# Kernel tuning notes

Measured on AMD Instinct MI355X. Metric: run time of the kernel, lower is better.

Reference implementation:

```python
import jax, jax.numpy as jnp
import numpy as np

B, L_SRC, L_TGT, H = 8, 256, 256, 768
N_SRC_WORDS, N_TGT_WORDS = 128, 128


def setup_inputs() -> dict:
    key = jax.random.key(0)
    k1, k2 = jax.random.split(key, 2)
    L = L_SRC + L_TGT
    tok_h = jax.random.normal(k1, (B, L, H), dtype=jnp.float32)
    attention_mask = jnp.ones((B, L), dtype=jnp.int32)
    # monotone word ids covering exactly N words (ragged spans of ~2 tokens/word)
    src_ids = (jnp.arange(L_SRC) * N_SRC_WORDS // L_SRC).astype(jnp.int64)
    tgt_ids = (jnp.arange(L_TGT) * N_TGT_WORDS // L_TGT).astype(jnp.int64)
    source_word_ids = jnp.broadcast_to(src_ids, (B, L_SRC))
    target_word_ids = jnp.broadcast_to(tgt_ids, (B, L_TGT))
    W = jax.random.normal(k2, (2 * H, 1), dtype=jnp.float32) * 0.02
    b = jnp.zeros((1,), dtype=jnp.float32)
    return dict(tok_h=tok_h, attention_mask=attention_mask,
                source_word_ids=source_word_ids, target_word_ids=target_word_ids,
                W=W, b=b, S=N_SRC_WORDS, T=N_TGT_WORDS)


def _pool_words(tok_h, combined_wid, attention_mask, n_words):
    """Vectorized equivalent of _pool_word_embeddings: mean over each
    contiguous run of equal word ids (masked / -1 tokens break runs)."""
    Bv, Lv, Hv = tok_h.shape
    valid = (attention_mask > 0) & (combined_wid >= 0)          # [B, L]
    prev_wid = jnp.pad(combined_wid[:, :-1], ((0, 0), (1, 0)), constant_values=-2)
    prev_valid = jnp.pad(valid[:, :-1], ((0, 0), (1, 0)), constant_values=False)
    new_run = valid & ((combined_wid != prev_wid) | (~prev_valid))
    run_id = jnp.cumsum(new_run.astype(jnp.int32), axis=1) - 1  # [B, L]
    n_seg = n_words + 1                                         # +1 dummy slot for invalid tokens
    seg = jnp.where(valid, run_id, n_words)
    gseg = (seg + jnp.arange(Bv, dtype=seg.dtype)[:, None] * n_seg).reshape(-1)
    sums = jax.ops.segment_sum(tok_h.reshape(Bv * Lv, Hv), gseg,
                               num_segments=Bv * n_seg).reshape(Bv, n_seg, Hv)
    counts = jax.ops.segment_sum(valid.astype(tok_h.dtype).reshape(-1), gseg,
                                 num_segments=Bv * n_seg).reshape(Bv, n_seg, 1)
    pooled = sums[:, :n_words] / jnp.maximum(counts[:, :n_words], 1.0)
    return pooled                                               # [B, n_words, H]


def reference(tok_h, attention_mask, source_word_ids, target_word_ids, W, b, S, T):
    combined_wid = jnp.concatenate([source_word_ids, target_word_ids], axis=1)  # [B, L]
    pooled = _pool_words(tok_h, combined_wid, attention_mask, S + T)            # [B, S+T, H]
    src = pooled[:, :S]            # [B, S, H]
    tgt = pooled[:, S:S + T]       # [B, T, H]
    # classifier(concat([src_exp, tgt_exp])) == src@W[:H] + tgt@W[H:] + b
    Hd = tok_h.shape[-1]
    w_src, w_tgt = W[:Hd, 0], W[Hd:, 0]
    logits = (src @ w_src)[:, :, None] + (tgt @ w_tgt)[:, None, :] + b[0]       # [B, S, T]
    return logits
```

## Files before the change

kernel.cpp:

```cpp
#include <hip/hip_runtime.h>
#include <hip/hip_bf16.h>

constexpr int B    = 8;
constexpr int LS   = 256;
constexpr int L    = 512;
constexpr int H    = 768;
constexpr int S    = 128;
constexpr int T    = 128;
constexpr int NW   = 256;
constexpr int NSEG = 513;

__global__ __launch_bounds__(64) void seg_count_kernel(
    const int* __restrict__ mask, const int* __restrict__ sw,
    const int* __restrict__ tw, int* __restrict__ seg,
    float* __restrict__ sums, float* __restrict__ cnts)
{
    const int b    = blockIdx.x;
    const int lane = threadIdx.x;

    __shared__ float lcnt[NSEG];
    for (int i = lane; i < NSEG; i += 64) lcnt[i] = 0.f;
    __syncthreads();

    const int base = lane * 8;
    int  wid[8]; bool val[8];
    #pragma unroll
    for (int j = 0; j < 8; ++j) {
        const int l = base + j;
        const int w = (l < LS) ? sw[b * LS + l] : tw[b * LS + (l - LS)];
        wid[j] = w;
        val[j] = (mask[b * L + l] > 0) && (w >= 0);
    }

    int pw = -2; bool pv = false;
    if (base > 0) {
        const int l = base - 1;
        pw = (l < LS) ? sw[b * LS + l] : tw[b * LS + (l - LS)];
        pv = (mask[b * L + l] > 0) && (pw >= 0);
    }

    int loc[8]; int c = 0;
    #pragma unroll
    for (int j = 0; j < 8; ++j) {
        const int nr = (val[j] && (wid[j] != pw || !pv)) ? 1 : 0;
        c += nr;
        loc[j] = c;
        pw = wid[j]; pv = val[j];
    }

    int inc = c;
    #pragma unroll
    for (int off = 1; off < 64; off <<= 1) {
        const int v = __shfl_up(inc, off);
        if (lane >= off) inc += v;
    }
    const int excl = inc - c;

    #pragma unroll
    for (int j = 0; j < 8; ++j) {
        const int rid = excl + loc[j] - 1;
        int sg = val[j] ? rid : NW;
        if (sg > NSEG - 1) sg = NSEG - 1;
        seg[b * L + base + j] = sg;
        atomicAdd(&lcnt[sg], 1.0f);
    }
    __syncthreads();

    for (int i = lane; i < NSEG; i += 64) {
        cnts[b * NSEG + i] = lcnt[i];
        sums[b * NSEG + i] = 0.f;
    }
}

__global__ __launch_bounds__(256) void dot_kernel(
    const float* __restrict__ tok, const float* __restrict__ Wp,
    const int* __restrict__ seg, float* __restrict__ sums)
{
    const int lane  = threadIdx.x & 63;
    const int wv    = threadIdx.x >> 6;
    const int token = blockIdx.x * 4 + wv;
    const int b     = token >> 9;

    const int sg = seg[token];
    if (sg >= NW) return;

    const float* wvec = Wp + ((sg < S) ? 0 : H);
    const float4* t4  = reinterpret_cast<const float4*>(tok + (size_t)token * H);
    const float4* w4  = reinterpret_cast<const float4*>(wvec);

    float acc = 0.f;
    #pragma unroll
    for (int k = 0; k < 3; ++k) {
        const float4 a = t4[lane + 64 * k];
        const float4 w = w4[lane + 64 * k];
        acc += a.x * w.x + a.y * w.y + a.z * w.z + a.w * w.w;
    }
    #pragma unroll
    for (int off = 32; off; off >>= 1) acc += __shfl_xor(acc, off);

    if (lane == 0) atomicAdd(&sums[b * NSEG + sg], acc);
}

__global__ __launch_bounds__(256) void logits_kernel(
    const float* __restrict__ sums, const float* __restrict__ cnts,
    const float* __restrict__ bias, float* __restrict__ out)
{
    const int b   = blockIdx.x;
    const int tid = threadIdx.x;

    __shared__ float ssrc[S], stgt[T];
    if (tid < S) {
        ssrc[tid] = sums[b * NSEG + tid] / fmaxf(cnts[b * NSEG + tid], 1.f);
    } else {
        const int j = tid - S;
        stgt[j] = sums[b * NSEG + S + j] / fmaxf(cnts[b * NSEG + S + j], 1.f);
    }
    __syncthreads();

    const float b0 = bias[0];
    const int i  = tid >> 1;
    const int jb = (tid & 1) * 64;
    const float si = ssrc[i] + b0;

    float4* o = reinterpret_cast<float4*>(out + (size_t)b * S * T + i * T + jb);
    #pragma unroll
    for (int j = 0; j < 64; j += 4) {
        float4 v;
        v.x = si + stgt[jb + j + 0];
        v.y = si + stgt[jb + j + 1];
        v.z = si + stgt[jb + j + 2];
        v.w = si + stgt[jb + j + 3];
        o[j >> 2] = v;
    }
}

extern "C" void kernel_launch(void* const* d_in, const int* in_sizes, int n_in,
                              void* d_out, int out_size, void* d_ws, size_t ws_size,
                              hipStream_t stream) {
    const float* tok  = (const float*)d_in[0];
    const int*   mask = (const int*)  d_in[1];
    const int*   sw   = (const int*)  d_in[2];
    const int*   tw   = (const int*)  d_in[3];
    const float* W    = (const float*)d_in[4];
    const float* bias = (const float*)d_in[5];
    float*       out  = (float*)d_out;

    float* sums = (float*)d_ws;
    float* cnts = sums + B * NSEG;
    int*   seg  = (int*)(cnts + B * NSEG);

    seg_count_kernel<<<B, 64, 0, stream>>>(mask, sw, tw, seg, sums, cnts);
    dot_kernel<<<(B * L) / 4, 256, 0, stream>>>(tok, W, seg, sums);
    logits_kernel<<<B, 256, 0, stream>>>(sums, cnts, bias, out);
}
```

Before: 16.90 us.

## Compute both weight dots per token and fuse segmentation into finalize kernel

The dot kernel no longer depends on segment ids. It computes each token's dot product against both the source and target weight halves and stores them as a float2. The segmentation scan, counting, pooling and logits are merged into one 1024-thread kernel per batch that uses shared-memory atomics. This removes one kernel launch and the global atomics, at the cost of a second dot product per token and an extra weight load.

```diff
diff --git a/kernel.cpp b/kernel.cpp
--- a/kernel.cpp
+++ b/kernel.cpp
@@ -8,128 +8,124 @@
 constexpr int S    = 128;
 constexpr int T    = 128;
 constexpr int NW   = 256;
-constexpr int NSEG = 513;
 
-__global__ __launch_bounds__(64) void seg_count_kernel(
-    const int* __restrict__ mask, const int* __restrict__ sw,
-    const int* __restrict__ tw, int* __restrict__ seg,
-    float* __restrict__ sums, float* __restrict__ cnts)
-{
-    const int b    = blockIdx.x;
-    const int lane = threadIdx.x;
-
-    __shared__ float lcnt[NSEG];
-    for (int i = lane; i < NSEG; i += 64) lcnt[i] = 0.f;
-    __syncthreads();
-
-    const int base = lane * 8;
-    int  wid[8]; bool val[8];
-    #pragma unroll
-    for (int j = 0; j < 8; ++j) {
-        const int l = base + j;
-        const int w = (l < LS) ? sw[b * LS + l] : tw[b * LS + (l - LS)];
-        wid[j] = w;
-        val[j] = (mask[b * L + l] > 0) && (w >= 0);
-    }
-
-    int pw = -2; bool pv = false;
-    if (base > 0) {
-        const int l = base - 1;
-        pw = (l < LS) ? sw[b * LS + l] : tw[b * LS + (l - LS)];
-        pv = (mask[b * L + l] > 0) && (pw >= 0);
-    }
-
-    int loc[8]; int c = 0;
-    #pragma unroll
-    for (int j = 0; j < 8; ++j) {
-        const int nr = (val[j] && (wid[j] != pw || !pv)) ? 1 : 0;
-        c += nr;
-        loc[j] = c;
-        pw = wid[j]; pv = val[j];
-    }
-
-    int inc = c;
-    #pragma unroll
-    for (int off = 1; off < 64; off <<= 1) {
-        const int v = __shfl_up(inc, off);
-        if (lane >= off) inc += v;
-    }
-    const int excl = inc - c;
-
-    #pragma unroll
-    for (int j = 0; j < 8; ++j) {
-        const int rid = excl + loc[j] - 1;
-        int sg = val[j] ? rid : NW;
-        if (sg > NSEG - 1) sg = NSEG - 1;
-        seg[b * L + base + j] = sg;
-        atomicAdd(&lcnt[sg], 1.0f);
-    }
-    __syncthreads();
-
-    for (int i = lane; i < NSEG; i += 64) {
-        cnts[b * NSEG + i] = lcnt[i];
-        sums[b * NSEG + i] = 0.f;
-    }
-}
-
-__global__ __launch_bounds__(256) void dot_kernel(
+__global__ __launch_bounds__(256) void dot2_kernel(
     const float* __restrict__ tok, const float* __restrict__ Wp,
-    const int* __restrict__ seg, float* __restrict__ sums)
+    float2* __restrict__ dvals)
 {
     const int lane  = threadIdx.x & 63;
     const int wv    = threadIdx.x >> 6;
     const int token = blockIdx.x * 4 + wv;
-    const int b     = token >> 9;
 
-    const int sg = seg[token];
-    if (sg >= NW) return;
+    const float4* t4 = reinterpret_cast<const float4*>(tok + (size_t)token * H);
+    const float4* s4 = reinterpret_cast<const float4*>(Wp);
+    const float4* g4 = reinterpret_cast<const float4*>(Wp + H);
 
-    const float* wvec = Wp + ((sg < S) ? 0 : H);
-    const float4* t4  = reinterpret_cast<const float4*>(tok + (size_t)token * H);
-    const float4* w4  = reinterpret_cast<const float4*>(wvec);
-
-    float acc = 0.f;
+    float as = 0.f, at = 0.f;
     #pragma unroll
     for (int k = 0; k < 3; ++k) {
         const float4 a = t4[lane + 64 * k];
-        const float4 w = w4[lane + 64 * k];
-        acc += a.x * w.x + a.y * w.y + a.z * w.z + a.w * w.w;
+        const float4 s = s4[lane + 64 * k];
+        const float4 g = g4[lane + 64 * k];
+        as += a.x * s.x + a.y * s.y + a.z * s.z + a.w * s.w;
+        at += a.x * g.x + a.y * g.y + a.z * g.z + a.w * g.w;
     }
     #pragma unroll
-    for (int off = 32; off; off >>= 1) acc += __shfl_xor(acc, off);
-
-    if (lane == 0) atomicAdd(&sums[b * NSEG + sg], acc);
+    for (int off = 32; off; off >>= 1) {
+        as += __shfl_xor(as, off);
+        at += __shfl_xor(at, off);
+    }
+    if (lane == 0) dvals[token] = make_float2(as, at);
 }
 
-__global__ __launch_bounds__(256) void logits_kernel(
-    const float* __restrict__ sums, const float* __restrict__ cnts,
+__global__ __launch_bounds__(1024) void finalize_kernel(
+    const int* __restrict__ mask, const int* __restrict__ sw,
+    const int* __restrict__ tw, const float2* __restrict__ dvals,
     const float* __restrict__ bias, float* __restrict__ out)
 {
     const int b   = blockIdx.x;
     const int tid = threadIdx.x;
 
-    __shared__ float ssrc[S], stgt[T];
-    if (tid < S) {
-        ssrc[tid] = sums[b * NSEG + tid] / fmaxf(cnts[b * NSEG + tid], 1.f);
-    } else {
-        const int j = tid - S;
-        stgt[j] = sums[b * NSEG + S + j] / fmaxf(cnts[b * NSEG + S + j], 1.f);
+    __shared__ int   sseg[L];
+    __shared__ float lsum[NW + 1];
+    __shared__ float lcnt[NW + 1];
+    __shared__ float pooled[NW];
+
+    if (tid < NW + 1) { lsum[tid] = 0.f; lcnt[tid] = 0.f; }
+    __syncthreads();
+
+    if (tid < 64) {
+        const int lane = tid;
+        const int base = lane * 8;
+
+        int  wid[8]; bool val[8];
+        #pragma unroll
+        for (int j = 0; j < 8; ++j) {
+            const int l = base + j;
+            const int w = (l < LS) ? sw[b * LS + l] : tw[b * LS + (l - LS)];
+            wid[j] = w;
+            val[j] = (mask[b * L + l] > 0) && (w >= 0);
+        }
+
+        int pw = -2; bool pv = false;
+        if (base > 0) {
+            const int l = base - 1;
+            pw = (l < LS) ? sw[b * LS + l] : tw[b * LS + (l - LS)];
+            pv = (mask[b * L + l] > 0) && (pw >= 0);
+        }
+
+        int loc[8]; int c = 0;
+        #pragma unroll
+        for (int j = 0; j < 8; ++j) {
+            const int nr = (val[j] && (wid[j] != pw || !pv)) ? 1 : 0;
+            c += nr;
+            loc[j] = c;
+            pw = wid[j]; pv = val[j];
+        }
+
+        int inc = c;
+        #pragma unroll
+        for (int off = 1; off < 64; off <<= 1) {
+            const int v = __shfl_up(inc, off);
+            if (lane >= off) inc += v;
+        }
+        const int excl = inc - c;
+
+        #pragma unroll
+        for (int j = 0; j < 8; ++j) {
+            const int rid = excl + loc[j] - 1;
+            const int sg  = (val[j] && rid < NW) ? rid : NW;
+            sseg[base + j] = sg;
+            atomicAdd(&lcnt[sg], 1.0f);
+        }
     }
     __syncthreads();
 
+    if (tid < L) {
+        const int sg = sseg[tid];
+        if (sg < NW) {
+            const float2 d = dvals[b * L + tid];
+            atomicAdd(&lsum[sg], (sg < S) ? d.x : d.y);
+        }
+    }
+    __syncthreads();
+
+    if (tid < NW) pooled[tid] = lsum[tid] / fmaxf(lcnt[tid], 1.f);
+    __syncthreads();
+
     const float b0 = bias[0];
-    const int i  = tid >> 1;
-    const int jb = (tid & 1) * 64;
-    const float si = ssrc[i] + b0;
+    const int i  = tid >> 3;
+    const int jb = (tid & 7) * 16;
+    const float si = pooled[i] + b0;
 
     float4* o = reinterpret_cast<float4*>(out + (size_t)b * S * T + i * T + jb);
     #pragma unroll
-    for (int j = 0; j < 64; j += 4) {
+    for (int j = 0; j < 16; j += 4) {
         float4 v;
-        v.x = si + stgt[jb + j + 0];
-        v.y = si + stgt[jb + j + 1];
-        v.z = si + stgt[jb + j + 2];
-        v.w = si + stgt[jb + j + 3];
+        v.x = si + pooled[S + jb + j + 0];
+        v.y = si + pooled[S + jb + j + 1];
+        v.z = si + pooled[S + jb + j + 2];
+        v.w = si + pooled[S + jb + j + 3];
         o[j >> 2] = v;
     }
 }
@@ -145,11 +141,8 @@
     const float* bias = (const float*)d_in[5];
     float*       out  = (float*)d_out;
 
-    float* sums = (float*)d_ws;
-    float* cnts = sums + B * NSEG;
-    int*   seg  = (int*)(cnts + B * NSEG);
+    float2* dvals = (float2*)d_ws;
 
-    seg_count_kernel<<<B, 64, 0, stream>>>(mask, sw, tw, seg, sums, cnts);
-    dot_kernel<<<(B * L) / 4, 256, 0, stream>>>(tok, W, seg, sums);
-    logits_kernel<<<B, 256, 0, stream>>>(sums, cnts, bias, out);
+    dot2_kernel<<<(B * L) / 4, 256, 0, stream>>>(tok, W, dvals);
+    finalize_kernel<<<B, 1024, 0, stream>>>(mask, sw, tw, dvals, bias, out);
 }
```

Result: faster. 15.56 us (-7.9%).
